# Kernel optimization log

Hardware: AMD Instinct MI355X
Metric: run time of the kernel (lower is better)

## Reference

```python
import jax, jax.numpy as jnp
import numpy as np

NHEAD = 8
NEG_INF = -1e9
LN_EPS = 1e-5


def setup_inputs() -> dict:
    key = jax.random.key(0)
    ks = jax.random.split(key, 8)
    B, Q, N, C = 2, 256, 16384, 256
    return {
        "queries": jax.random.normal(ks[0], (B, Q, C), jnp.float32),
        "vid_features": jax.random.normal(ks[1], (B, C, N), jnp.float32),
        "vid_mask": jax.random.uniform(ks[2], (B, Q, N), jnp.float32),
        "pos_embed": jax.random.normal(ks[3], (B, C, N), jnp.float32),
        "query_embed": jax.random.normal(ks[4], (B, Q, C), jnp.float32),
        "in_proj_w": jax.random.normal(ks[5], (3 * C, C), jnp.float32) * 0.02,
        "in_proj_b": jnp.zeros((3 * C,), jnp.float32),
        "out_proj_w": jax.random.normal(ks[6], (C, C), jnp.float32) * 0.02,
        "out_proj_b": jnp.zeros((C,), jnp.float32),
        "ln_gamma": jnp.ones((C,), jnp.float32),
        "ln_beta": jnp.zeros((C,), jnp.float32),
    }


def reference(queries, vid_features, vid_mask, pos_embed, query_embed,
              in_proj_w, in_proj_b, out_proj_w, out_proj_b, ln_gamma, ln_beta):
    B, Q, C = queries.shape
    H = NHEAD
    d = C // H

    vf = jnp.transpose(vid_features, (0, 2, 1))   # B N C
    pe = jnp.transpose(pos_embed, (0, 2, 1))      # B N C

    q_in = queries + query_embed                  # with_pos_embed on queries
    k_in = vf + pe                                # with_pos_embed on keys
    v_in = vf

    wq, wk, wv = jnp.split(in_proj_w, 3, axis=0)
    bq, bk, bv = jnp.split(in_proj_b, 3)

    q = (q_in @ wq.T + bq).reshape(B, Q, H, d)
    k = (k_in @ wk.T + bk).reshape(B, -1, H, d)
    v = (v_in @ wv.T + bv).reshape(B, -1, H, d)

    scale = 1.0 / jnp.sqrt(jnp.asarray(d, q.dtype))
    logits = jnp.einsum('bqhd,bnhd->bhqn', q, k) * scale  # B H Q N

    # Hard masking: block keys where mask prob < 0.5; if a query row is
    # fully blocked, fall back to unmasked attention (avoid NaN softmax).
    blocked = vid_mask < 0.5                                 # B Q N
    all_blocked = jnp.all(blocked, axis=-1, keepdims=True)   # B Q 1
    blocked = blocked & jnp.logical_not(all_blocked)
    logits = jnp.where(blocked[:, None, :, :], NEG_INF, logits)

    attn = jax.nn.softmax(logits, axis=-1)
    ctx = jnp.einsum('bhqn,bnhd->bqhd', attn, v).reshape(B, Q, C)
    tgt2 = ctx @ out_proj_w.T + out_proj_b

    # residual + LayerNorm (dropout p=0.0 -> identity)
    x = queries + tgt2
    mu = jnp.mean(x, axis=-1, keepdims=True)
    var = jnp.mean(jnp.square(x - mu), axis=-1, keepdims=True)
    return (x - mu) / jnp.sqrt(var + LN_EPS) * ln_gamma + ln_beta
```

## Files before the change

kernel.cpp:

```cpp
#include <hip/hip_runtime.h>
#include <stdint.h>

#define B_ 2
#define Q_ 256
#define N_ 16384
#define C_ 256
#define H_ 8
#define D_ 32
#define NC_ 32
#define SCALEQ 0.2550542176432015f

typedef __bf16 bf16x8 __attribute__((ext_vector_type(8)));
typedef float f32x4 __attribute__((ext_vector_type(4)));

__device__ __forceinline__ uint16_t bfbits(float f) {
  union { __bf16 h; uint16_t u; } c; c.h = (__bf16)f; return c.u;
}
__device__ __forceinline__ float bf2f(uint16_t u) {
  union { uint32_t u; float f; } c; c.u = (uint32_t)u << 16;
  return c.f;
}
__device__ __forceinline__ uint32_t pk2(float a, float b) {
  union { struct { uint16_t lo, hi; } s; uint32_t u; } c;
  c.s.lo = bfbits(a); c.s.hi = bfbits(b);
  return c.u;
}
__device__ __forceinline__ void lgkm0_barrier() {
  __builtin_amdgcn_sched_barrier(0);
  asm volatile("s_waitcnt lgkmcnt(0)" ::: "memory");
  __builtin_amdgcn_sched_barrier(0);
  __builtin_amdgcn_s_barrier();
  __builtin_amdgcn_sched_barrier(0);
}

__global__ __launch_bounds__(256) void prep(const float* __restrict__ inw,
                                            const float* __restrict__ outw,
                                            const float* __restrict__ vm,
                                            uint16_t* __restrict__ wb,
                                            float* __restrict__ woT,
                                            uint32_t* __restrict__ mb) {
  __shared__ __align__(16) char sh[4352];
  const int bid = blockIdx.x;
  const int t = threadIdx.x;
  if (bid < 96) {
    const int i = (bid * 256 + t) * 8;
    const float4 a = *reinterpret_cast<const float4*>(inw + i);
    const float4 b = *reinterpret_cast<const float4*>(inw + i + 4);
    ushort4 lo = {bfbits(a.x), bfbits(a.y), bfbits(a.z), bfbits(a.w)};
    ushort4 hi = {bfbits(b.x), bfbits(b.y), bfbits(b.z), bfbits(b.w)};
    *reinterpret_cast<ushort4*>(wb + i) = lo;
    *reinterpret_cast<ushort4*>(wb + i + 4) = hi;
  } else if (bid < 160) {
    float(*s)[33] = reinterpret_cast<float(*)[33]>(sh);
    const int bb = bid - 96;
    const int bx = bb & 7, by = bb >> 3;
    const int r0 = by * 32, c0 = bx * 32;
    const int tr = t >> 5, tc = t & 31;
#pragma unroll
    for (int k = 0; k < 4; ++k)
      s[tr + 8 * k][tc] = outw[(size_t)(r0 + tr + 8 * k) * 256 + c0 + tc];
    __syncthreads();
#pragma unroll
    for (int k = 0; k < 4; ++k)
      woT[(size_t)(c0 + tr + 8 * k) * 256 + r0 + tc] = s[tc][tr + 8 * k];
  } else {
    uint8_t(*nib)[256] = reinterpret_cast<uint8_t(*)[256]>(sh);
    __shared__ int wcnt[4];
    __shared__ int tot;
    const int bq = bid - 160;
    const float* row = vm + (size_t)bq * N_;
    const int lane = t & 63;
    int cnt = 0;
#pragma unroll
    for (int i = 0; i < 16; ++i) {
      const float4 v = *reinterpret_cast<const float4*>(&row[i * 1024 + 4 * t]);
      const uint32_t nb = (v.x < 0.5f ? 1u : 0u) | (v.y < 0.5f ? 2u : 0u) |
                          (v.z < 0.5f ? 4u : 0u) | (v.w < 0.5f ? 8u : 0u);
      nib[i][t] = (uint8_t)nb;
      cnt += __popc(nb);
    }
    for (int o = 32; o > 0; o >>= 1) cnt += __shfl_down(cnt, o, 64);
    if (lane == 0) wcnt[t >> 6] = cnt;
    __syncthreads();
    if (t == 0) tot = wcnt[0] + wcnt[1] + wcnt[2] + wcnt[3];
    __syncthreads();
    const bool allb = (tot == N_);
    uint32_t* dst = mb + (size_t)bq * 512;
#pragma unroll
    for (int k = 0; k < 2; ++k) {
      const int w = k * 256 + t;
      const int i = w >> 5, tw = w & 31;
      const uint2 u = *reinterpret_cast<const uint2*>(&nib[i][8 * tw]);
      uint32_t y0 = u.x & 0x0F0F0F0Fu; y0 = y0 | (y0 >> 4);
      uint32_t y1 = u.y & 0x0F0F0F0Fu; y1 = y1 | (y1 >> 4);
      const uint32_t word = (y0 & 0xFFu) | (((y0 >> 16) & 0xFFu) << 8) |
                            ((y1 & 0xFFu) << 16) | (((y1 >> 16) & 0xFFu) << 24);
      dst[w] = allb ? 0u : word;
    }
  }
}

__global__ __launch_bounds__(1024, 4) void kvqproj(const float* __restrict__ vf,
                                                   const float* __restrict__ pe,
                                                   const float* __restrict__ queries,
                                                   const float* __restrict__ qembed,
                                                   const uint16_t* __restrict__ wkv,
                                                   const float* __restrict__ bias,
                                                   uint16_t* __restrict__ Kh,
                                                   uint16_t* __restrict__ Vh,
                                                   uint16_t* __restrict__ Qb) {
  __shared__ __align__(16) uint16_t shp[2][2][128][40];
  const int bid = blockIdx.x;
  const int t = threadIdx.x, wid = t >> 6, lane = t & 63;
  const int g = lane >> 4, c15 = lane & 15;

  if (bid >= 8) {
    const int kb = bid - 8;
    const int b = kb >> 7, nt = kb & 127;
    const int n0 = nt * 128;
    const bool isK = wid < 8;
    const int w = wid & 7;

    const uint16_t* Wsec = wkv + (size_t)((isK ? 256 : 512) + w * 32 + c15) * C_;

    f32x4 acc[16];
    if (isK) {
#pragma unroll
      for (int cf = 0; cf < 2; ++cf) {
        f32x4 iv;
#pragma unroll
        for (int j = 0; j < 4; ++j) iv[j] = bias[256 + w * 32 + cf * 16 + 4 * g + j];
#pragma unroll
        for (int nf = 0; nf < 8; ++nf) acc[cf * 8 + nf] = iv;
      }
    } else {
#pragma unroll
      for (int cf = 0; cf < 2; ++cf) {
        const float bv = bias[512 + w * 32 + cf * 16 + c15];
        const f32x4 iv = {bv, bv, bv, bv};
#pragma unroll
        for (int nf = 0; nf < 8; ++nf) acc[nf * 2 + cf] = iv;
      }
    }

    const int cp = t >> 6, n2 = lane;
    const float* Xb = vf + ((size_t)b * C_ + 2 * cp) * N_ + n0 + 2 * n2;
    const float* Pb = pe + ((size_t)b * C_ + 2 * cp) * N_ + n0 + 2 * n2;
    const int cps = cp ^ (((n2 >> 2) & 3) << 2);

    float2 xA0, xA1, pA0, pA1, xB0, xB1, pB0, pB1;
    bf16x8 W[2];

#define LOADW(s)                                                             \
    {                                                                        \
      _Pragma("unroll") for (int cf = 0; cf < 2; ++cf)                       \
          W[cf] = *(const bf16x8*)(Wsec + (size_t)cf * 16 * C_ + (s) * 32 + g * 8); \
    }
#define LOADA(X0, X1, P0, P1, s)                                             \
    {                                                                        \
      const float* x_ = Xb + (size_t)(s) * 32 * N_;                          \
      const float* p_ = Pb + (size_t)(s) * 32 * N_;                          \
      X0 = *(const float2*)x_;                                               \
      X1 = *(const float2*)(x_ + N_);                                        \
      P0 = *(const float2*)p_;                                               \
      P1 = *(const float2*)(p_ + N_);                                        \
    }
#define WRITEA(X0, X1, P0, P1, buf)                                          \
    {                                                                        \
      *(uint32_t*)&shp[0][buf][2 * n2][2 * cps]     = pk2(X0.x + P0.x, X1.x + P1.x); \
      *(uint32_t*)&shp[0][buf][2 * n2 + 1][2 * cps] = pk2(X0.y + P0.y, X1.y + P1.y); \
      *(uint32_t*)&shp[1][buf][2 * n2][2 * cps]     = pk2(X0.x, X1.x);       \
      *(uint32_t*)&shp[1][buf][2 * n2 + 1][2 * cps] = pk2(X0.y, X1.y);       \
    }
#define COMPUTE(buf)                                                         \
    {                                                                        \
      _Pragma("unroll") for (int nf = 0; nf < 8; ++nf) {                     \
        const int r_ = nf * 16 + c15;                                        \
        const int o_ = (g ^ ((r_ >> 3) & 3)) * 8;                            \
        if (isK) {                                                           \
          const bf16x8 Fp = *(const bf16x8*)&shp[0][buf][r_][o_];            \
          _Pragma("unroll") for (int cf = 0; cf < 2; ++cf)                   \
              acc[cf * 8 + nf] = __builtin_amdgcn_mfma_f32_16x16x32_bf16(    \
                  W[cf], Fp, acc[cf * 8 + nf], 0, 0, 0);                     \
        } else {                                                             \
          const bf16x8 Fv = *(const bf16x8*)&shp[1][buf][r_][o_];            \
          _Pragma("unroll") for (int cf = 0; cf < 2; ++cf)                   \
              acc[nf * 2 + cf] = __builtin_amdgcn_mfma_f32_16x16x32_bf16(    \
                  Fv, W[cf], acc[nf * 2 + cf], 0, 0, 0);                     \
        }                                                                    \
      }                                                                      \
    }

    LOADA(xA0, xA1, pA0, pA1, 0);
    LOADA(xB0, xB1, pB0, pB1, 1);
    LOADW(0); WRITEA(xA0, xA1, pA0, pA1, 0); LOADA(xA0, xA1, pA0, pA1, 2);
    lgkm0_barrier(); COMPUTE(0); __builtin_amdgcn_sched_barrier(0);
    LOADW(1); WRITEA(xB0, xB1, pB0, pB1, 1); LOADA(xB0, xB1, pB0, pB1, 3);
    lgkm0_barrier(); COMPUTE(1); __builtin_amdgcn_sched_barrier(0);
    LOADW(2); WRITEA(xA0, xA1, pA0, pA1, 0); LOADA(xA0, xA1, pA0, pA1, 4);
    lgkm0_barrier(); COMPUTE(0); __builtin_amdgcn_sched_barrier(0);
    LOADW(3); WRITEA(xB0, xB1, pB0, pB1, 1); LOADA(xB0, xB1, pB0, pB1, 5);
    lgkm0_barrier(); COMPUTE(1); __builtin_amdgcn_sched_barrier(0);
    LOADW(4); WRITEA(xA0, xA1, pA0, pA1, 0); LOADA(xA0, xA1, pA0, pA1, 6);
    lgkm0_barrier(); COMPUTE(0); __builtin_amdgcn_sched_barrier(0);
    LOADW(5); WRITEA(xB0, xB1, pB0, pB1, 1); LOADA(xB0, xB1, pB0, pB1, 7);
    lgkm0_barrier(); COMPUTE(1); __builtin_amdgcn_sched_barrier(0);
    LOADW(6); WRITEA(xA0, xA1, pA0, pA1, 0);
    lgkm0_barrier(); COMPUTE(0); __builtin_amdgcn_sched_barrier(0);
    LOADW(7); WRITEA(xB0, xB1, pB0, pB1, 1);
    lgkm0_barrier(); COMPUTE(1); __builtin_amdgcn_sched_barrier(0);

#undef LOADW
#undef LOADA
#undef WRITEA
#undef COMPUTE

    if (isK) {
      uint16_t* Kp = Kh + (size_t)(b * H_ + w) * N_ * D_;
#pragma unroll
      for (int cf = 0; cf < 2; ++cf)
#pragma unroll
        for (int nf = 0; nf < 8; ++nf) {
          const f32x4 a = acc[cf * 8 + nf];
          uint2 pkv;
          pkv.x = pk2(a[0], a[1]);
          pkv.y = pk2(a[2], a[3]);
          *(uint2*)&Kp[(size_t)(n0 + nf * 16 + c15) * D_ + cf * 16 + 4 * g] = pkv;
        }
    } else {
      uint16_t* Vp = Vh + (size_t)(b * H_ + w) * D_ * N_;
#pragma unroll
      for (int nf = 0; nf < 8; ++nf)
#pragma unroll
        for (int cf = 0; cf < 2; ++cf) {
          const f32x4 a = acc[nf * 2 + cf];
          uint2 pkv;
          pkv.x = pk2(a[0], a[1]);
          pkv.y = pk2(a[2], a[3]);
          *(uint2*)&Vp[(size_t)(cf * 16 + c15) * N_ + n0 + nf * 16 + 4 * g] = pkv;
        }
    }
  } else {
    uint16_t(*qv)[64][40] = reinterpret_cast<uint16_t(*)[64][40]>(&shp[0][0][0][0]);
    const int qb = bid;
    const int q0g = qb * 64;
    const int b = q0g >> 8, q0 = q0g & 255;
    if (t < 512) {
      const int r = t >> 3, c0 = (t & 7) * 32, s = t & 7;
      const float* Qrow = queries + (size_t)(q0g + r) * C_ + c0;
      const float* Erow = qembed + (size_t)(q0g + r) * C_ + c0;
#pragma unroll
      for (int ph = 0; ph < 2; ++ph) {
        float4 a4[4], e4[4];
#pragma unroll
        for (int k = 0; k < 4; ++k) a4[k] = reinterpret_cast<const float4*>(Qrow + ph * 16)[k];
#pragma unroll
        for (int k = 0; k < 4; ++k) e4[k] = reinterpret_cast<const float4*>(Erow + ph * 16)[k];
        const float* af = reinterpret_cast<const float*>(a4);
        const float* ef = reinterpret_cast<const float*>(e4);
#pragma unroll
        for (int i = 0; i < 16; ++i) {
          const int cl = ph * 16 + i;
          const int col = cl ^ (8 * ((r >> 3) & 3));
          qv[s][r][col] = bfbits(af[i] + ef[i]);
        }
        __builtin_amdgcn_sched_barrier(0);
      }
    }
    lgkm0_barrier();
    if (t < 512) {
      const int w = wid;
      f32x4 acc[4][2];
#pragma unroll
      for (int nf = 0; nf < 2; ++nf) {
        const float bv = bias[w * 32 + nf * 16 + c15];
        const f32x4 iv = {bv, bv, bv, bv};
#pragma unroll
        for (int qf = 0; qf < 4; ++qf) acc[qf][nf] = iv;
      }
#pragma unroll
      for (int s8 = 0; s8 < 8; ++s8) {
        bf16x8 Bf[2];
#pragma unroll
        for (int nf = 0; nf < 2; ++nf)
          Bf[nf] = *reinterpret_cast<const bf16x8*>(
              wkv + (size_t)(w * 32 + nf * 16 + c15) * C_ + s8 * 32 + g * 8);
#pragma unroll
        for (int qf = 0; qf < 4; ++qf) {
          const int rr = qf * 16 + c15;
          const bf16x8 Af = *reinterpret_cast<const bf16x8*>(
              &qv[s8][rr][8 * (g ^ ((rr >> 3) & 3))]);
#pragma unroll
          for (int nf = 0; nf < 2; ++nf)
            acc[qf][nf] = __builtin_amdgcn_mfma_f32_16x16x32_bf16(Af, Bf[nf], acc[qf][nf], 0, 0, 0);
        }
      }
#pragma unroll
      for (int qf = 0; qf < 4; ++qf)
#pragma unroll
        for (int nf = 0; nf < 2; ++nf)
#pragma unroll
          for (int j = 0; j < 4; ++j) {
            const int q = q0 + qf * 16 + 4 * g + j;
            const int dk = nf * 16 + c15;
            Qb[((size_t)(b * H_ + w) * Q_ + q) * D_ + dk] = bfbits(acc[qf][nf][j] * SCALEQ);
          }
    }
  }
}

__global__ __launch_bounds__(512) void attn(const uint16_t* __restrict__ Qb,
                                            const uint16_t* __restrict__ Kh,
                                            const uint16_t* __restrict__ Vh,
                                            const uint32_t* __restrict__ mb,
                                            uint16_t* __restrict__ ctx_part,
                                            float* __restrict__ lsum_part) {
  const int bid = blockIdx.x;
  const int nc = bid & 31, h = (bid >> 5) & 7, b = bid >> 8;
  const int t = threadIdx.x, wid = t >> 6, lane = t & 63;
  const int g = lane >> 4, c15 = lane & 15;
  const int qw0 = wid * 32;
  const int nbase = nc * (N_ / NC_);
  constexpr int SS = (N_ / NC_) / 128;

  __shared__ __align__(16) uint16_t kst[2][128][40];
  __shared__ __align__(16) uint16_t vst[2][32][136];
  __shared__ __align__(16) uint16_t plds[8][32][40];

  const uint16_t* Qp = Qb + (size_t)(b * H_ + h) * Q_ * D_;
  bf16x8 qfr[2];
#pragma unroll
  for (int qf = 0; qf < 2; ++qf)
    qfr[qf] = *reinterpret_cast<const bf16x8*>(Qp + (size_t)(qw0 + qf * 16 + c15) * D_ + g * 8);

  f32x4 acc[2][2];
  const f32x4 zero4 = {0.f, 0.f, 0.f, 0.f};
#pragma unroll
  for (int qf = 0; qf < 2; ++qf)
#pragma unroll
    for (int dvf = 0; dvf < 2; ++dvf) acc[qf][dvf] = zero4;
  float lsum[2][4] = {};

  const uint32_t* mrow = mb + (size_t)b * Q_ * (N_ / 32);

  const int krow = t >> 2, kch = t & 3;
  const uint16_t* ksrc = Kh + ((size_t)(b * H_ + h) * N_ + nbase + krow) * 32 + kch * 8;
  const int vrow = t >> 4, vch = t & 15;
  const uint16_t* vsrc = Vh + ((size_t)(b * H_ + h) * 32 + vrow) * N_ + nbase + vch * 8;

  uint4 kreg = *(const uint4*)ksrc;
  uint4 vreg = *(const uint4*)vsrc;

  int cur = 0;
  for (int ss = 0; ss < SS; ++ss) {
    *(uint4*)&kst[cur][krow][kch * 8] = kreg;
    *(uint4*)&vst[cur][vrow][vch * 8] = vreg;
    if (ss < SS - 1) {
      kreg = *(const uint4*)(ksrc + (size_t)(ss + 1) * 128 * 32);
      vreg = *(const uint4*)(vsrc + (ss + 1) * 128);
    }
    lgkm0_barrier();

    const int nstart = nbase + ss * 128;
#pragma unroll
    for (int half = 0; half < 2; ++half) {
      uint32_t mw[2][4][2];
#pragma unroll
      for (int qf = 0; qf < 2; ++qf)
#pragma unroll
        for (int j = 0; j < 4; ++j) {
          const int q = qw0 + qf * 16 + 4 * g + j;
          const uint2 u = *reinterpret_cast<const uint2*>(
              &mrow[(size_t)q * (N_ / 32) + (nstart >> 5) + half * 2]);
          mw[qf][j][0] = u.x;
          mw[qf][j][1] = u.y;
        }
#pragma unroll
      for (int s2 = 0; s2 < 2; ++s2) {
        const int sub = half * 2 + s2;
        const int nl0 = sub * 32;
        bf16x8 kfr[2];
#pragma unroll
        for (int nf = 0; nf < 2; ++nf)
          kfr[nf] = *reinterpret_cast<const bf16x8*>(&kst[cur][nl0 + nf * 16 + c15][g * 8]);
        f32x4 s[2][2];
#pragma unroll
        for (int qf = 0; qf < 2; ++qf)
#pragma unroll
          for (int nf = 0; nf < 2; ++nf)
            s[qf][nf] = __builtin_amdgcn_mfma_f32_16x16x32_bf16(qfr[qf], kfr[nf], zero4, 0, 0, 0);

#pragma unroll
        for (int qf = 0; qf < 2; ++qf) {
#pragma unroll
          for (int j = 0; j < 4; ++j) {
            const uint32_t wmask = mw[qf][j][s2];
#pragma unroll
            for (int nf = 0; nf < 2; ++nf) {
              const int bit = nf * 16 + c15;
              const float p = ((wmask >> bit) & 1u) ? 0.0f : exp2f(s[qf][nf][j]);
              lsum[qf][j] += p;
              plds[wid][qf * 16 + 4 * g + j][nf * 16 + c15] = bfbits(p);
            }
          }
        }
        __asm__ volatile("s_waitcnt lgkmcnt(0)" ::: "memory");
#pragma unroll
        for (int qf = 0; qf < 2; ++qf) {
          const bf16x8 pa = *reinterpret_cast<const bf16x8*>(&plds[wid][qf * 16 + c15][g * 8]);
#pragma unroll
          for (int dvf = 0; dvf < 2; ++dvf) {
            const bf16x8 vb =
                *reinterpret_cast<const bf16x8*>(&vst[cur][dvf * 16 + c15][nl0 + g * 8]);
            acc[qf][dvf] = __builtin_amdgcn_mfma_f32_16x16x32_bf16(pa, vb, acc[qf][dvf], 0, 0, 0);
          }
        }
      }
    }
    __builtin_amdgcn_sched_barrier(0);
    cur ^= 1;
  }

#pragma unroll
  for (int qf = 0; qf < 2; ++qf)
#pragma unroll
    for (int j = 0; j < 4; ++j) {
      float v = lsum[qf][j];
      v += __shfl_xor(v, 1, 64);
      v += __shfl_xor(v, 2, 64);
      v += __shfl_xor(v, 4, 64);
      v += __shfl_xor(v, 8, 64);
      lsum[qf][j] = v;
    }

#pragma unroll
  for (int qf = 0; qf < 2; ++qf)
#pragma unroll
    for (int dvf = 0; dvf < 2; ++dvf)
#pragma unroll
      for (int j = 0; j < 4; ++j) {
        const int q = qw0 + qf * 16 + 4 * g + j;
        const size_t base = (((size_t)(b * Q_ + q) * H_ + h) * NC_ + nc) * D_;
        ctx_part[base + dvf * 16 + c15] = bfbits(acc[qf][dvf][j]);
      }
  if (c15 == 0) {
#pragma unroll
    for (int qf = 0; qf < 2; ++qf)
#pragma unroll
      for (int j = 0; j < 4; ++j) {
        const int q = qw0 + qf * 16 + 4 * g + j;
        lsum_part[((size_t)(b * Q_ + q) * H_ + h) * NC_ + nc] = lsum[qf][j];
      }
  }
}

__global__ __launch_bounds__(256) void epilogue(const uint16_t* __restrict__ ctx_part,
                                                const float* __restrict__ lsum_part,
                                                const float* __restrict__ queries,
                                                const float* __restrict__ woT,
                                                const float* __restrict__ bo,
                                                const float* __restrict__ gamma,
                                                const float* __restrict__ beta,
                                                float* __restrict__ out) {
  const int bq = blockIdx.x;
  const int t = threadIdx.x;
  const int h = t >> 5, dv = t & 31;
  const uint16_t* crow = ctx_part + (size_t)bq * H_ * NC_ * D_;
  const float* lrow = lsum_part + (size_t)bq * H_ * NC_;
  float cs = 0.f, ls = 0.f;
#pragma unroll 8
  for (int k = 0; k < NC_; ++k) {
    cs += bf2f(crow[((size_t)h * NC_ + k) * D_ + dv]);
    ls += lrow[h * NC_ + k];
  }
  __shared__ float ctxrow[C_];
  ctxrow[t] = cs / ls;
  __syncthreads();
  float acc = bo[t];
#pragma unroll 8
  for (int j = 0; j < C_; ++j) acc = fmaf(ctxrow[j], woT[(size_t)j * C_ + t], acc);
  const float x = queries[(size_t)bq * C_ + t] + acc;
  float s1 = x, s2 = x * x;
  for (int o = 32; o > 0; o >>= 1) {
    s1 += __shfl_down(s1, o, 64);
    s2 += __shfl_down(s2, o, 64);
  }
  __shared__ float r1[4], r2[4];
  if ((t & 63) == 0) { r1[t >> 6] = s1; r2[t >> 6] = s2; }
  __syncthreads();
  const float mu = (r1[0] + r1[1] + r1[2] + r1[3]) * (1.0f / C_);
  const float e2 = (r2[0] + r2[1] + r2[2] + r2[3]) * (1.0f / C_);
  const float var = e2 - mu * mu;
  out[(size_t)bq * C_ + t] = (x - mu) * rsqrtf(var + 1e-5f) * gamma[t] + beta[t];
}

extern "C" void kernel_launch(void* const* d_in, const int* in_sizes, int n_in,
                              void* d_out, int out_size, void* d_ws, size_t ws_size,
                              hipStream_t stream) {
  const float* queries    = (const float*)d_in[0];
  const float* vidfeat    = (const float*)d_in[1];
  const float* vidmask    = (const float*)d_in[2];
  const float* posembed   = (const float*)d_in[3];
  const float* queryembed = (const float*)d_in[4];
  const float* inw        = (const float*)d_in[5];
  const float* inb        = (const float*)d_in[6];
  const float* outw       = (const float*)d_in[7];
  const float* outb       = (const float*)d_in[8];
  const float* gamma      = (const float*)d_in[9];
  const float* beta       = (const float*)d_in[10];
  float* out = (float*)d_out;

  char* ws = (char*)d_ws;
  size_t off = 0;
  uint16_t* Qb   = (uint16_t*)(ws + off); off += (size_t)B_ * H_ * Q_ * D_ * 2;
  uint16_t* Kh   = (uint16_t*)(ws + off); off += (size_t)B_ * H_ * N_ * D_ * 2;
  uint16_t* Vh   = (uint16_t*)(ws + off); off += (size_t)B_ * H_ * D_ * N_ * 2;
  uint32_t* mb   = (uint32_t*)(ws + off); off += (size_t)B_ * Q_ * (N_ / 32) * 4;
  uint16_t* wkv  = (uint16_t*)(ws + off); off += (size_t)768 * C_ * 2;
  float* woT     = (float*)(ws + off);    off += (size_t)C_ * C_ * 4;
  uint16_t* ctxp = (uint16_t*)(ws + off); off += (size_t)B_ * Q_ * H_ * NC_ * D_ * 2;
  float* lsump   = (float*)(ws + off);    off += (size_t)B_ * Q_ * H_ * NC_ * 4;

  prep<<<dim3(672), dim3(256), 0, stream>>>(inw, outw, vidmask, wkv, woT, mb);
  kvqproj<<<dim3(264), dim3(1024), 0, stream>>>(vidfeat, posembed, queries, queryembed,
                                                wkv, inb, Kh, Vh, Qb);
  attn<<<dim3(B_ * H_ * NC_), dim3(512), 0, stream>>>(Qb, Kh, Vh, mb, ctxp, lsump);
  epilogue<<<dim3(B_ * Q_), dim3(256), 0, stream>>>(ctxp, lsump, queries, woT, outb,
                                                    gamma, beta, out);
}
```

Before: 89.82 us.

## Compute transposed scores and pass P to PV MFMA via lane shuffles instead of LDS

```diff
diff --git a/kernel.cpp b/kernel.cpp
--- a/kernel.cpp
+++ b/kernel.cpp
@@ -325,7 +325,6 @@
 
   __shared__ __align__(16) uint16_t kst[2][128][40];
   __shared__ __align__(16) uint16_t vst[2][32][136];
-  __shared__ __align__(16) uint16_t plds[8][32][40];
 
   const uint16_t* Qp = Qb + (size_t)(b * H_ + h) * Q_ * D_;
   bf16x8 qfr[2];
@@ -339,7 +338,7 @@
   for (int qf = 0; qf < 2; ++qf)
 #pragma unroll
     for (int dvf = 0; dvf < 2; ++dvf) acc[qf][dvf] = zero4;
-  float lsum[2][4] = {};
+  float lsum[2] = {0.f, 0.f};
 
   const uint32_t* mrow = mb + (size_t)b * Q_ * (N_ / 32);
 
@@ -350,6 +349,10 @@
 
   uint4 kreg = *(const uint4*)ksrc;
   uint4 vreg = *(const uint4*)vsrc;
+
+  const int srcA = c15 + (g & 1) * 32;
+  const int srcB = srcA + 16;
+  const bool hiSel = g >= 2;
 
   int cur = 0;
   for (int ss = 0; ss < SS; ++ss) {
@@ -364,17 +367,15 @@
     const int nstart = nbase + ss * 128;
 #pragma unroll
     for (int half = 0; half < 2; ++half) {
-      uint32_t mw[2][4][2];
-#pragma unroll
-      for (int qf = 0; qf < 2; ++qf)
-#pragma unroll
-        for (int j = 0; j < 4; ++j) {
-          const int q = qw0 + qf * 16 + 4 * g + j;
-          const uint2 u = *reinterpret_cast<const uint2*>(
-              &mrow[(size_t)q * (N_ / 32) + (nstart >> 5) + half * 2]);
-          mw[qf][j][0] = u.x;
-          mw[qf][j][1] = u.y;
-        }
+      uint32_t mw2[2][2];
+#pragma unroll
+      for (int qf = 0; qf < 2; ++qf) {
+        const int q = qw0 + qf * 16 + c15;
+        const uint2 u = *reinterpret_cast<const uint2*>(
+            &mrow[(size_t)q * (N_ / 32) + (nstart >> 5) + half * 2]);
+        mw2[qf][0] = u.x;
+        mw2[qf][1] = u.y;
+      }
 #pragma unroll
       for (int s2 = 0; s2 < 2; ++s2) {
         const int sub = half * 2 + s2;
@@ -388,31 +389,39 @@
         for (int qf = 0; qf < 2; ++qf)
 #pragma unroll
           for (int nf = 0; nf < 2; ++nf)
-            s[qf][nf] = __builtin_amdgcn_mfma_f32_16x16x32_bf16(qfr[qf], kfr[nf], zero4, 0, 0, 0);
+            s[qf][nf] = __builtin_amdgcn_mfma_f32_16x16x32_bf16(kfr[nf], qfr[qf], zero4, 0, 0, 0);
 
 #pragma unroll
         for (int qf = 0; qf < 2; ++qf) {
-#pragma unroll
-          for (int j = 0; j < 4; ++j) {
-            const uint32_t wmask = mw[qf][j][s2];
-#pragma unroll
-            for (int nf = 0; nf < 2; ++nf) {
-              const int bit = nf * 16 + c15;
-              const float p = ((wmask >> bit) & 1u) ? 0.0f : exp2f(s[qf][nf][j]);
-              lsum[qf][j] += p;
-              plds[wid][qf * 16 + 4 * g + j][nf * 16 + c15] = bfbits(p);
+          const uint32_t wm = mw2[qf][s2];
+          float p[2][4];
+#pragma unroll
+          for (int nf = 0; nf < 2; ++nf)
+#pragma unroll
+            for (int j = 0; j < 4; ++j) {
+              const int bit = nf * 16 + 4 * g + j;
+              const float pv = ((wm >> bit) & 1u) ? 0.0f : exp2f(s[qf][nf][j]);
+              p[nf][j] = pv;
+              lsum[qf] += pv;
             }
-          }
-        }
-        __asm__ volatile("s_waitcnt lgkmcnt(0)" ::: "memory");
-#pragma unroll
-        for (int qf = 0; qf < 2; ++qf) {
-          const bf16x8 pa = *reinterpret_cast<const bf16x8*>(&plds[wid][qf * 16 + c15][g * 8]);
+          const uint32_t d0 = pk2(p[0][0], p[0][1]);
+          const uint32_t d1 = pk2(p[0][2], p[0][3]);
+          const uint32_t d2 = pk2(p[1][0], p[1][1]);
+          const uint32_t d3 = pk2(p[1][2], p[1][3]);
+          const uint32_t a0 = __shfl((int)d0, srcA, 64), a2 = __shfl((int)d2, srcA, 64);
+          const uint32_t b0 = __shfl((int)d1, srcA, 64), b2 = __shfl((int)d3, srcA, 64);
+          const uint32_t c0 = __shfl((int)d0, srcB, 64), c2 = __shfl((int)d2, srcB, 64);
+          const uint32_t e0 = __shfl((int)d1, srcB, 64), e2 = __shfl((int)d3, srcB, 64);
+          union { uint32_t u[4]; bf16x8 v; } pa;
+          pa.u[0] = hiSel ? a2 : a0;
+          pa.u[1] = hiSel ? b2 : b0;
+          pa.u[2] = hiSel ? c2 : c0;
+          pa.u[3] = hiSel ? e2 : e0;
 #pragma unroll
           for (int dvf = 0; dvf < 2; ++dvf) {
             const bf16x8 vb =
                 *reinterpret_cast<const bf16x8*>(&vst[cur][dvf * 16 + c15][nl0 + g * 8]);
-            acc[qf][dvf] = __builtin_amdgcn_mfma_f32_16x16x32_bf16(pa, vb, acc[qf][dvf], 0, 0, 0);
+            acc[qf][dvf] = __builtin_amdgcn_mfma_f32_16x16x32_bf16(pa.v, vb, acc[qf][dvf], 0, 0, 0);
           }
         }
       }
@@ -422,16 +431,12 @@
   }
 
 #pragma unroll
-  for (int qf = 0; qf < 2; ++qf)
-#pragma unroll
-    for (int j = 0; j < 4; ++j) {
-      float v = lsum[qf][j];
-      v += __shfl_xor(v, 1, 64);
-      v += __shfl_xor(v, 2, 64);
-      v += __shfl_xor(v, 4, 64);
-      v += __shfl_xor(v, 8, 64);
-      lsum[qf][j] = v;
-    }
+  for (int qf = 0; qf < 2; ++qf) {
+    float v = lsum[qf];
+    v += __shfl_xor(v, 16, 64);
+    v += __shfl_xor(v, 32, 64);
+    lsum[qf] = v;
+  }
 
 #pragma unroll
   for (int qf = 0; qf < 2; ++qf)
@@ -443,14 +448,12 @@
         const size_t base = (((size_t)(b * Q_ + q) * H_ + h) * NC_ + nc) * D_;
         ctx_part[base + dvf * 16 + c15] = bfbits(acc[qf][dvf][j]);
       }
-  if (c15 == 0) {
-#pragma unroll
-    for (int qf = 0; qf < 2; ++qf)
-#pragma unroll
-      for (int j = 0; j < 4; ++j) {
-        const int q = qw0 + qf * 16 + 4 * g + j;
-        lsum_part[((size_t)(b * Q_ + q) * H_ + h) * NC_ + nc] = lsum[qf][j];
-      }
+  if (lane < 16) {
+#pragma unroll
+    for (int qf = 0; qf < 2; ++qf) {
+      const int q = qw0 + qf * 16 + c15;
+      lsum_part[((size_t)(b * Q_ + q) * H_ + h) * NC_ + nc] = lsum[qf];
+    }
   }
 }
 
```

Result: slower. 93.55 us (+4.2%).
